# Kernel optimization log

Measured on AMD Instinct MI355X. Metric: run time of the kernel, lower is better.

Reference implementation:

```python
import jax, jax.numpy as jnp
from jax import lax
import numpy as np

EPS = 1e-6

def layer_norm(x, scale, bias):
    mu = jnp.mean(x, axis=-1, keepdims=True)
    var = jnp.var(x, axis=-1, keepdims=True)
    y = (x - mu) * lax.rsqrt(var + EPS)
    if scale is not None:
        y = y * scale
    if bias is not None:
        y = y + bias
    return y

def mha(keys, values, queries, mask, head_count):
    # keys/values: [B, K, E]; queries: [B, Q, E]; mask: [B, K] (1 = attend)
    B, Q, E = queries.shape
    d = E // head_count
    q = queries.reshape(B, Q, head_count, d) / jnp.asarray(d ** 0.5, queries.dtype)
    k = keys.reshape(B, -1, head_count, d)
    v = values.reshape(B, -1, head_count, d)
    bias = (1.0 - mask.astype(q.dtype)) * -1e12  # [B, K]
    w = jnp.einsum('bqhc,bkhc->bhqk', q, k) + bias[:, None, None, :]
    w = jax.nn.softmax(w, axis=-1)
    out = jnp.einsum('bhqk,bkhc->bqhc', w, v)
    return out.reshape(B, Q, E)

def setup_inputs() -> dict:
    key = jax.random.key(0)
    ks = jax.random.split(key, 16)
    B, T, E, G, I = 64, 64, 2048, 4096, 256
    s = 0.02
    inp = {
        'decoder_state': jax.random.normal(ks[0], (B, 1, E), jnp.float32),
        'encoder_state': jax.random.normal(ks[1], (B, T, E), jnp.float32),
        'attention_state': jnp.zeros((2 * B, I, E), jnp.float32),
        'attention_mask': jnp.ones((B, T), jnp.int32),
        'token_index': 100,
        # params
        'ln_pre_sa_b': jnp.zeros((E,), jnp.float32),
        'q_sa': s * jax.random.normal(ks[2], (E, E), jnp.float32),
        'k_sa': s * jax.random.normal(ks[3], (E, E), jnp.float32),
        'v_sa': s * jax.random.normal(ks[4], (E, E), jnp.float32),
        'o_sa': s * jax.random.normal(ks[5], (E, E), jnp.float32),
        'ln_sa_s': jnp.ones((E,), jnp.float32),
        'ln_sa_b': jnp.zeros((E,), jnp.float32),
        'ln_pre_ca_b': jnp.zeros((E,), jnp.float32),
        'q_ca': s * jax.random.normal(ks[6], (E, E), jnp.float32),
        'k_ca': s * jax.random.normal(ks[7], (E, E), jnp.float32),
        'v_ca': s * jax.random.normal(ks[8], (E, E), jnp.float32),
        'o_ca': s * jax.random.normal(ks[9], (E, E), jnp.float32),
        'ln_ca_s': jnp.ones((E,), jnp.float32),
        'ln_ca_b': jnp.zeros((E,), jnp.float32),
        'glu_ln0_b': jnp.zeros((E,), jnp.float32),
        'fc0_w': s * jax.random.normal(ks[10], (E, G), jnp.float32),
        'fc1_w': s * jax.random.normal(ks[11], (E, G), jnp.float32),
        'glu_ln1_s': jnp.ones((G,), jnp.float32),
        'glu_ln1_b': jnp.zeros((G,), jnp.float32),
        'fc2_w': s * jax.random.normal(ks[12], (G, E), jnp.float32),
    }
    return inp

IMAGE_TOKEN_COUNT = 256
HEAD_COUNT = 32

def reference(decoder_state, encoder_state, attention_state,
              ln_pre_sa_b, q_sa, k_sa, v_sa, o_sa, ln_sa_s, ln_sa_b,
              ln_pre_ca_b, q_ca, k_ca, v_ca, o_ca, ln_ca_s, ln_ca_b,
              glu_ln0_b, fc0_w, fc1_w, glu_ln1_s, glu_ln1_b, fc2_w,
              attention_mask, token_index):
    B = decoder_state.shape[0]
    # --- self attention (pre-norm, KV cache update) ---
    residual = decoder_state
    x = layer_norm(decoder_state, None, ln_pre_sa_b)
    self_mask = jnp.tile(jnp.arange(IMAGE_TOKEN_COUNT) < token_index + 1, (B, 1))
    keys = x @ k_sa
    values = x @ v_sa
    queries = x @ q_sa
    attention_state = lax.dynamic_update_slice(
        attention_state, jnp.concatenate([keys, values]).astype(jnp.float32),
        (0, token_index, 0))
    cached_k = attention_state[:B]
    cached_v = attention_state[B:]
    x = (mha(cached_k, cached_v, queries, self_mask, HEAD_COUNT) @ o_sa).astype(decoder_state.dtype)
    x = layer_norm(x, ln_sa_s, ln_sa_b)
    decoder_state = residual + x
    # --- cross attention ---
    residual = decoder_state
    x = layer_norm(decoder_state, None, ln_pre_ca_b)
    ek = encoder_state @ k_ca
    ev = encoder_state @ v_ca
    q = x @ q_ca
    x = mha(ek, ev, q, attention_mask, HEAD_COUNT) @ o_ca
    x = layer_norm(x, ln_ca_s, ln_ca_b)
    decoder_state = residual + x
    # --- GLU FFN ---
    residual = decoder_state
    z = layer_norm(decoder_state, None, glu_ln0_b)
    w = jax.nn.gelu(z @ fc0_w, approximate=False)
    v = z @ fc1_w
    z = layer_norm(w * v, glu_ln1_s, glu_ln1_b) @ fc2_w
    decoder_state = residual + z
    return decoder_state, attention_state
```

## Files before the change

kernel.cpp:

```cpp
#include <hip/hip_runtime.h>

#define Bb   64
#define Ee   2048
#define Tt   64
#define Gg   4096
#define Ii   256
#define Hh   32
#define Dd   64

using f32x4_t  = __attribute__((ext_vector_type(4))) float;
using bf16x8_t = __attribute__((ext_vector_type(8))) __bf16;

__device__ __forceinline__ unsigned short f2bf(float f) {
  unsigned u = __float_as_uint(f);
  u += 0x7FFFu + ((u >> 16) & 1u);
  return (unsigned short)(u >> 16);
}
__device__ __forceinline__ float ldkv(float v) { return v; }
__device__ __forceinline__ float ldkv(unsigned short v) {
  return __uint_as_float(((unsigned)v) << 16);
}
__device__ __forceinline__ float gelu_f(float x) {
  return 0.5f * x * (1.0f + erff(x * 0.70710678118654752f));
}

template <typename T> __device__ __forceinline__ float4 ld4(const T* p);
template <> __device__ __forceinline__ float4 ld4<float>(const float* p) {
  return *(const float4*)p;
}
template <> __device__ __forceinline__ float4 ld4<unsigned short>(const unsigned short* p) {
  ushort4 u = *(const ushort4*)p;
  return make_float4(ldkv(u.x), ldkv(u.y), ldkv(u.z), ldkv(u.w));
}

__global__ void copy_state_k(const float4* __restrict__ src, float4* __restrict__ dst,
                             const float4* __restrict__ kb, const float4* __restrict__ vb,
                             const int* __restrict__ tokp) {
  const int t = *tokp;
  const long n4 = (long)128 * Ii * (Ee / 4);
  long i = (long)blockIdx.x * blockDim.x + threadIdx.x;
  const long stride = (long)gridDim.x * blockDim.x;
  for (; i < n4; i += stride) {
    long row = i >> 9;
    int tt = (int)(row & (Ii - 1));
    float4 v;
    if (tt == t) {
      int bh  = (int)(row >> 8);
      int col = (int)(i & 511);
      const float4* s = (bh < Bb) ? kb : vb;
      v = s[(long)(bh & (Bb - 1)) * (Ee / 4) + col];
    } else {
      v = src[i];
    }
    dst[i] = v;
  }
}

__global__ void conv_bf16_k(const float4* __restrict__ in, unsigned short* __restrict__ out, long n4) {
  long i = (long)blockIdx.x * blockDim.x + threadIdx.x;
  long stride = (long)gridDim.x * blockDim.x;
  for (; i < n4; i += stride) {
    float4 f = in[i];
    ushort4 u;
    u.x = f2bf(f.x); u.y = f2bf(f.y); u.z = f2bf(f.z); u.w = f2bf(f.w);
    *(ushort4*)(out + i * 4) = u;
  }
}

__global__ void transpose_bf16_k(const float* __restrict__ W, unsigned short* __restrict__ Wt,
                                 int K, int N) {
  __shared__ unsigned short tile[64][65];
  int k0 = blockIdx.x * 64, n0 = blockIdx.y * 64;
  int c = threadIdx.x & 63;
  int r4 = threadIdx.x >> 6;
  #pragma unroll
  for (int i = 0; i < 16; i++) {
    int r = r4 + i * 4;
    tile[r][c] = f2bf(W[(long)(k0 + r) * N + n0 + c]);
  }
  __syncthreads();
  #pragma unroll
  for (int i = 0; i < 16; i++) {
    int r = r4 + i * 4;
    Wt[(long)(n0 + r) * K + k0 + c] = tile[c][r];
  }
}

template <bool GELU, bool HAS_SCALE, bool HAS_RES, bool DUAL>
__global__ void ln_k(const float4* __restrict__ in1, const float4* __restrict__ in2,
                     const float* __restrict__ scale, const float* __restrict__ bias,
                     const float4* __restrict__ res,
                     float4* __restrict__ out1, float4* __restrict__ out2) {
  const int row = blockIdx.x, tid = threadIdx.x;
  const int C = blockDim.x * 4;
  const long base = (long)row * blockDim.x + tid;

  float4 p = in1[base];
  if (GELU) {
    float4 vv = in2[base];
    p.x = gelu_f(p.x) * vv.x; p.y = gelu_f(p.y) * vv.y;
    p.z = gelu_f(p.z) * vv.z; p.w = gelu_f(p.w) * vv.w;
  }
  float s  = p.x + p.y + p.z + p.w;
  float s2 = p.x * p.x + p.y * p.y + p.z * p.z + p.w * p.w;

  __shared__ float rs[16], rs2[16];
  int lane = tid & 63, w = tid >> 6;
  #pragma unroll
  for (int o = 32; o; o >>= 1) { s += __shfl_down(s, o, 64); s2 += __shfl_down(s2, o, 64); }
  if (lane == 0) { rs[w] = s; rs2[w] = s2; }
  __syncthreads();
  if (tid == 0) {
    float ts = 0.f, ts2 = 0.f;
    int nw = blockDim.x >> 6;
    for (int i = 0; i < nw; i++) { ts += rs[i]; ts2 += rs2[i]; }
    float mu = ts / C;
    float var = ts2 / C - mu * mu;
    rs[0]  = mu;
    rs2[0] = rsqrtf(var + 1e-6f);
  }
  __syncthreads();
  const float mu = rs[0], rstd = rs2[0];

  float4 o;
  o.x = (p.x - mu) * rstd; o.y = (p.y - mu) * rstd;
  o.z = (p.z - mu) * rstd; o.w = (p.w - mu) * rstd;
  if (HAS_SCALE) {
    float4 sc4 = ((const float4*)scale)[tid];
    o.x *= sc4.x; o.y *= sc4.y; o.z *= sc4.z; o.w *= sc4.w;
  }
  float4 b4 = ((const float4*)bias)[tid];
  o.x += b4.x; o.y += b4.y; o.z += b4.z; o.w += b4.w;
  if (HAS_RES) {
    float4 r4 = res[base];
    o.x += r4.x; o.y += r4.y; o.z += r4.z; o.w += r4.w;
  }
  out1[base] = o;
  if (DUAL) out2[base] = o;
}

template <int NW>
__global__ __launch_bounds__(256)
void proj_k(const float* __restrict__ X,
            const float* __restrict__ W0, const float* __restrict__ W1,
            const float* __restrict__ W2,
            float* __restrict__ P, int K, int N) {
  __shared__ float Xs[64 * 64];
  const int nq = threadIdx.x & 31;
  const int m0 = (threadIdx.x >> 5) * 8;
  const int n  = blockIdx.x * 128 + nq * 4;
  const int kbase = blockIdx.y * 128;

  f32x4_t acc[NW][8];
  #pragma unroll
  for (int wsel = 0; wsel < NW; wsel++)
    #pragma unroll
    for (int i = 0; i < 8; i++) acc[wsel][i] = (f32x4_t){0.f, 0.f, 0.f, 0.f};

  for (int k0 = kbase; k0 < kbase + 128; k0 += 64) {
    __syncthreads();
    #pragma unroll
    for (int j = 0; j < 16; j++) {
      int e = threadIdx.x + j * 256;
      Xs[e] = X[(long)(e >> 6) * K + k0 + (e & 63)];
    }
    __syncthreads();
    #pragma unroll 4
    for (int kk = 0; kk < 64; kk++) {
      const long wrow = (long)(k0 + kk) * N + n;
      f32x4_t w4[NW];
      w4[0] = *(const f32x4_t*)(W0 + wrow);
      if (NW > 1) w4[1] = *(const f32x4_t*)(W1 + wrow);
      if (NW > 2) w4[2] = *(const f32x4_t*)(W2 + wrow);
      #pragma unroll
      for (int i = 0; i < 8; i++) {
        float xm = Xs[(m0 + i) * 64 + kk];
        #pragma unroll
        for (int wsel = 0; wsel < NW; wsel++) acc[wsel][i] += xm * w4[wsel];
      }
    }
  }
  float* base = P + (long)blockIdx.y * ((long)NW * 64 * N);
  #pragma unroll
  for (int wsel = 0; wsel < NW; wsel++) {
    #pragma unroll
    for (int i = 0; i < 8; i++) {
      *(f32x4_t*)(base + ((long)wsel * 64 + m0 + i) * N + n) = acc[wsel][i];
    }
  }
}

template <bool ACCUM>
__global__ void reduce_k(const float4* __restrict__ P, float4* __restrict__ Y,
                         int KB, long n4) {
  long i = (long)blockIdx.x * blockDim.x + threadIdx.x;
  if (i >= n4) return;
  float4 s = ACCUM ? Y[i] : make_float4(0.f, 0.f, 0.f, 0.f);
  for (int k = 0; k < KB; k++) {
    float4 p = P[(long)k * n4 + i];
    s.x += p.x; s.y += p.y; s.z += p.z; s.w += p.w;
  }
  Y[i] = s;
}

template <typename KVT>
__global__ void attn_k(const float* __restrict__ Q, const KVT* __restrict__ Kc,
                       const KVT* __restrict__ Vc, float* __restrict__ O,
                       const int* __restrict__ tokp, const int* __restrict__ maskp,
                       int L, long bstride, float scale) {
  const int b = blockIdx.x, h = blockIdx.y;
  const int lane = threadIdx.x;
  __shared__ float sc[256];
  const float* qp = Q + (long)b * Ee + h * Dd;
  const int n = tokp ? (*tokp + 1) : L;

  float mx = -3.0e38f;
  for (int pos = lane; pos < n; pos += 64) {
    bool valid = maskp ? (maskp[(long)b * L + pos] != 0) : true;
    float s = -1.0e30f;
    if (valid) {
      const KVT* kr = Kc + (long)b * bstride + (long)pos * Ee + h * Dd;
      float acc = 0.f;
      #pragma unroll
      for (int j = 0; j < 16; j++) {
        float4 kv = ld4(kr + j * 4);
        acc += qp[j*4+0]*kv.x + qp[j*4+1]*kv.y + qp[j*4+2]*kv.z + qp[j*4+3]*kv.w;
      }
      s = acc * scale;
    }
    sc[pos] = s;
    mx = fmaxf(mx, s);
  }
  __syncthreads();
  #pragma unroll
  for (int o = 32; o; o >>= 1) mx = fmaxf(mx, __shfl_down(mx, o, 64));
  mx = __shfl(mx, 0, 64);

  float sum = 0.f;
  for (int pos = lane; pos < n; pos += 64) {
    float e = expf(sc[pos] - mx);
    sc[pos] = e;
    sum += e;
  }
  __syncthreads();
  #pragma unroll
  for (int o = 32; o; o >>= 1) sum += __shfl_down(sum, o, 64);
  sum = __shfl(sum, 0, 64);
  const float inv = 1.0f / sum;

  const KVT* vbase = Vc + (long)b * bstride + h * Dd + lane;
  float acc = 0.f;
  int pos = 0;
  for (; pos + 8 <= n; pos += 8) {
    #pragma unroll
    for (int u = 0; u < 8; u++)
      acc += sc[pos + u] * ldkv(vbase[(long)(pos + u) * Ee]);
  }
  for (; pos < n; pos++) acc += sc[pos] * ldkv(vbase[(long)pos * Ee]);
  O[(long)b * Ee + h * Dd + lane] = acc * inv;
}

__global__ __launch_bounds__(256)
void gemm_bf16_k(const unsigned short* __restrict__ A, const unsigned short* __restrict__ Bt,
                 unsigned short* __restrict__ C, int M, int N, int K) {
  __shared__ unsigned short As[128 * 32];
  __shared__ unsigned short Bs[128 * 32];
  const int m0 = blockIdx.x * 128;
  const int n0 = blockIdx.y * 128;
  const int tid  = threadIdx.x;
  const int lane = tid & 63;
  const int wave = tid >> 6;
  const int wm = (wave >> 1) * 64;
  const int wn = (wave & 1) * 64;
  const int fr = lane & 15;
  const int fq = lane >> 4;

  const int r0 = tid >> 2;
  const int g0 = tid & 3;
  const int so1 = r0 * 32 + ((g0 ^ ((r0 >> 1) & 3)) * 8);
  const int so2 = so1 + 64 * 32;

  f32x4_t acc[4][4];
  const f32x4_t zero = {0.f, 0.f, 0.f, 0.f};
  #pragma unroll
  for (int i = 0; i < 4; i++)
    #pragma unroll
    for (int j = 0; j < 4; j++) acc[i][j] = zero;

  const long aR1 = (long)(m0 + r0) * K;
  const long aR2 = (long)(m0 + r0 + 64) * K;
  const long bR1 = (long)(n0 + r0) * K;
  const long bR2 = (long)(n0 + r0 + 64) * K;

  for (int k0 = 0; k0 < K; k0 += 32) {
    uint4 va1 = *(const uint4*)(A  + aR1 + k0 + g0 * 8);
    uint4 va2 = *(const uint4*)(A  + aR2 + k0 + g0 * 8);
    uint4 vb1 = *(const uint4*)(Bt + bR1 + k0 + g0 * 8);
    uint4 vb2 = *(const uint4*)(Bt + bR2 + k0 + g0 * 8);
    __syncthreads();
    *(uint4*)(As + so1) = va1;
    *(uint4*)(As + so2) = va2;
    *(uint4*)(Bs + so1) = vb1;
    *(uint4*)(Bs + so2) = vb2;
    __syncthreads();

    bf16x8_t af[4], bb[4];
    #pragma unroll
    for (int ms = 0; ms < 4; ms++) {
      int row = wm + ms * 16 + fr;
      af[ms] = __builtin_bit_cast(bf16x8_t,
               *(const uint4*)(As + row * 32 + ((fq ^ ((row >> 1) & 3)) * 8)));
    }
    #pragma unroll
    for (int ns = 0; ns < 4; ns++) {
      int row = wn + ns * 16 + fr;
      bb[ns] = __builtin_bit_cast(bf16x8_t,
               *(const uint4*)(Bs + row * 32 + ((fq ^ ((row >> 1) & 3)) * 8)));
    }
    #pragma unroll
    for (int ms = 0; ms < 4; ms++)
      #pragma unroll
      for (int ns = 0; ns < 4; ns++)
        acc[ms][ns] = __builtin_amdgcn_mfma_f32_16x16x32_bf16(af[ms], bb[ns], acc[ms][ns], 0, 0, 0);
  }

  #pragma unroll
  for (int ms = 0; ms < 4; ms++) {
    #pragma unroll
    for (int ns = 0; ns < 4; ns++) {
      int row = m0 + wm + ms * 16 + fq * 4;
      int col = n0 + wn + ns * 16 + fr;
      #pragma unroll
      for (int r = 0; r < 4; r++)
        C[(long)(row + r) * N + col] = f2bf(acc[ms][ns][r]);
    }
  }
}

extern "C" void kernel_launch(void* const* d_in, const int* in_sizes, int n_in,
                              void* d_out, int out_size, void* d_ws, size_t ws_size,
                              hipStream_t stream) {
  const float* dec    = (const float*)d_in[0];
  const float* enc    = (const float*)d_in[1];
  const float* astate = (const float*)d_in[2];
  const int*   amask  = (const int*)d_in[3];
  const int*   tokp   = (const int*)d_in[4];
  const float* ln_pre_sa_b = (const float*)d_in[5];
  const float* q_sa = (const float*)d_in[6];
  const float* k_sa = (const float*)d_in[7];
  const float* v_sa = (const float*)d_in[8];
  const float* o_sa = (const float*)d_in[9];
  const float* ln_sa_s = (const float*)d_in[10];
  const float* ln_sa_b = (const float*)d_in[11];
  const float* ln_pre_ca_b = (const float*)d_in[12];
  const float* q_ca = (const float*)d_in[13];
  const float* k_ca = (const float*)d_in[14];
  const float* v_ca = (const float*)d_in[15];
  const float* o_ca = (const float*)d_in[16];
  const float* ln_ca_s = (const float*)d_in[17];
  const float* ln_ca_b = (const float*)d_in[18];
  const float* glu_ln0_b = (const float*)d_in[19];
  const float* fc0 = (const float*)d_in[20];
  const float* fc1 = (const float*)d_in[21];
  const float* glu_ln1_s = (const float*)d_in[22];
  const float* glu_ln1_b = (const float*)d_in[23];
  const float* fc2 = (const float*)d_in[24];

  float* out_dec   = (float*)d_out;
  float* out_state = out_dec + (long)Bb * Ee;

  float* qb  = (float*)d_ws;
  float* kb  = qb  + 131072;
  float* vb  = kb  + 131072;
  float* ob  = vb  + 131072;
  float* q2  = ob  + 131072;
  float* ob2 = q2  + 131072;
  float* w0  = ob2 + 131072;
  float* v1  = w0  + 262144;
  float* x1  = v1  + 262144;
  float* ab  = x1  + 131072;
  float* ds2 = ab  + 131072;
  float* x3  = ds2 + 131072;
  float* cb  = x3  + 131072;
  float* ds3 = cb  + 131072;
  float* zb  = ds3 + 131072;
  float* wvn = zb  + 131072;
  unsigned short* ebf = (unsigned short*)(wvn + 262144);
  unsigned short* kt  = ebf + 8388608;
  unsigned short* vt  = kt  + 4194304;
  unsigned short* ekb = vt  + 4194304;
  unsigned short* evb = ekb + 8388608;
  float* arena = (float*)(evb + 8388608);

  conv_bf16_k<<<2048, 256, 0, stream>>>((const float4*)enc, ebf, (long)Bb * Tt * Ee / 4);
  transpose_bf16_k<<<dim3(32, 32), 256, 0, stream>>>(k_ca, kt, Ee, Ee);
  transpose_bf16_k<<<dim3(32, 32), 256, 0, stream>>>(v_ca, vt, Ee, Ee);
  gemm_bf16_k<<<dim3(32, 16), 256, 0, stream>>>(ebf, kt, ekb, 4096, Ee, Ee);
  gemm_bf16_k<<<dim3(32, 16), 256, 0, stream>>>(ebf, vt, evb, 4096, Ee, Ee);

  ln_k<false,false,false,false><<<Bb, 512, 0, stream>>>(
      (const float4*)dec, nullptr, nullptr, ln_pre_sa_b, nullptr, (float4*)x1, nullptr);
  proj_k<3><<<dim3(16, 16), 256, 0, stream>>>(x1, q_sa, k_sa, v_sa, arena, Ee, Ee);
  reduce_k<false><<<384, 256, 0, stream>>>((const float4*)arena, (float4*)qb, 16, 98304);
  copy_state_k<<<4096, 256, 0, stream>>>((const float4*)astate, (float4*)out_state,
                                         (const float4*)kb, (const float4*)vb, tokp);
  attn_k<float><<<dim3(Bb, Hh), 64, 0, stream>>>(qb, out_state,
      out_state + (long)Bb * Ii * Ee, ab, tokp, nullptr, Ii, (long)Ii * Ee, 0.125f);
  proj_k<1><<<dim3(16, 16), 256, 0, stream>>>(ab, o_sa, nullptr, nullptr, arena, Ee, Ee);
  reduce_k<false><<<128, 256, 0, stream>>>((const float4*)arena, (float4*)ob, 16, 32768);
  ln_k<false,true,true,false><<<Bb, 512, 0, stream>>>(
      (const float4*)ob, nullptr, ln_sa_s, ln_sa_b, (const float4*)dec, (float4*)ds2, nullptr);

  ln_k<false,false,false,false><<<Bb, 512, 0, stream>>>(
      (const float4*)ds2, nullptr, nullptr, ln_pre_ca_b, nullptr, (float4*)x3, nullptr);
  proj_k<1><<<dim3(16, 16), 256, 0, stream>>>(x3, q_ca, nullptr, nullptr, arena, Ee, Ee);
  reduce_k<false><<<128, 256, 0, stream>>>((const float4*)arena, (float4*)q2, 16, 32768);
  attn_k<unsigned short><<<dim3(Bb, Hh), 64, 0, stream>>>(q2, ekb, evb, cb,
      nullptr, amask, Tt, (long)Tt * Ee, 0.125f);
  proj_k<1><<<dim3(16, 16), 256, 0, stream>>>(cb, o_ca, nullptr, nullptr, arena, Ee, Ee);
  reduce_k<false><<<128, 256, 0, stream>>>((const float4*)arena, (float4*)ob2, 16, 32768);
  ln_k<false,true,true,true><<<Bb, 512, 0, stream>>>(
      (const float4*)ob2, nullptr, ln_ca_s, ln_ca_b, (const float4*)ds2,
      (float4*)ds3, (float4*)out_dec);

  ln_k<false,false,false,false><<<Bb, 512, 0, stream>>>(
      (const float4*)ds3, nullptr, nullptr, glu_ln0_b, nullptr, (float4*)zb, nullptr);
  proj_k<2><<<dim3(32, 16), 256, 0, stream>>>(zb, fc0, fc1, nullptr, arena, Ee, Gg);
  reduce_k<false><<<512, 256, 0, stream>>>((const float4*)arena, (float4*)w0, 16, 131072);
  ln_k<true,true,false,false><<<Bb, 1024, 0, stream>>>(
      (const float4*)w0, (const float4*)v1, glu_ln1_s, glu_ln1_b, nullptr, (float4*)wvn, nullptr);
  proj_k<1><<<dim3(16, 32), 256, 0, stream>>>(wvn, fc2, nullptr, nullptr, arena, Gg, Ee);
  reduce_k<true><<<128, 256, 0, stream>>>((const float4*)arena, (float4*)out_dec, 32, 32768);
}
```

Baseline: 1.067 ms.

## Fuse prep, split-K reductions and layernorms; merge dual bf16 GEMM with LDS-direct loads

Merges the encoder bf16 conversion and both weight transposes into one prep kernel. The K and V encoder GEMMs now run as a single launch that stages tiles with global_load_lds direct-to-LDS loads and no swizzle. Split-K reductions are folded into the state copy, the attention query load, and combined reduce+LN+residual+LN and reduce+GELU+LN kernels. The aim is to cut launch count and intermediate global round-trips, at the risk of LDS bank conflicts in the unswizzled GEMM and smaller per-block parallelism in the reductions.

```diff
diff --git a/kernel.cpp b/kernel.cpp
--- a/kernel.cpp
+++ b/kernel.cpp
@@ -23,6 +23,11 @@
 __device__ __forceinline__ float gelu_f(float x) {
   return 0.5f * x * (1.0f + erff(x * 0.70710678118654752f));
 }
+__device__ __forceinline__ void gld16(const void* g, void* l) {
+  __builtin_amdgcn_global_load_lds(
+      (const __attribute__((address_space(1))) unsigned int*)g,
+      (__attribute__((address_space(3))) unsigned int*)l, 16, 0, 0);
+}
 
 template <typename T> __device__ __forceinline__ float4 ld4(const T* p);
 template <> __device__ __forceinline__ float4 ld4<float>(const float* p) {
@@ -33,74 +38,115 @@
   return make_float4(ldkv(u.x), ldkv(u.y), ldkv(u.z), ldkv(u.w));
 }
 
-__global__ void copy_state_k(const float4* __restrict__ src, float4* __restrict__ dst,
-                             const float4* __restrict__ kb, const float4* __restrict__ vb,
-                             const int* __restrict__ tokp) {
-  const int t = *tokp;
-  const long n4 = (long)128 * Ii * (Ee / 4);
-  long i = (long)blockIdx.x * blockDim.x + threadIdx.x;
-  const long stride = (long)gridDim.x * blockDim.x;
-  for (; i < n4; i += stride) {
-    long row = i >> 9;
-    int tt = (int)(row & (Ii - 1));
-    float4 v;
-    if (tt == t) {
-      int bh  = (int)(row >> 8);
-      int col = (int)(i & 511);
-      const float4* s = (bh < Bb) ? kb : vb;
-      v = s[(long)(bh & (Bb - 1)) * (Ee / 4) + col];
-    } else {
-      v = src[i];
-    }
-    dst[i] = v;
-  }
-}
-
-__global__ void conv_bf16_k(const float4* __restrict__ in, unsigned short* __restrict__ out, long n4) {
-  long i = (long)blockIdx.x * blockDim.x + threadIdx.x;
-  long stride = (long)gridDim.x * blockDim.x;
-  for (; i < n4; i += stride) {
-    float4 f = in[i];
-    ushort4 u;
-    u.x = f2bf(f.x); u.y = f2bf(f.y); u.z = f2bf(f.z); u.w = f2bf(f.w);
-    *(ushort4*)(out + i * 4) = u;
-  }
-}
-
-__global__ void transpose_bf16_k(const float* __restrict__ W, unsigned short* __restrict__ Wt,
-                                 int K, int N) {
-  __shared__ unsigned short tile[64][65];
-  int k0 = blockIdx.x * 64, n0 = blockIdx.y * 64;
-  int c = threadIdx.x & 63;
-  int r4 = threadIdx.x >> 6;
-  #pragma unroll
-  for (int i = 0; i < 16; i++) {
-    int r = r4 + i * 4;
-    tile[r][c] = f2bf(W[(long)(k0 + r) * N + n0 + c]);
-  }
-  __syncthreads();
-  #pragma unroll
-  for (int i = 0; i < 16; i++) {
-    int r = r4 + i * 4;
-    Wt[(long)(n0 + r) * K + k0 + c] = tile[c][r];
-  }
-}
-
-template <bool GELU, bool HAS_SCALE, bool HAS_RES, bool DUAL>
-__global__ void ln_k(const float4* __restrict__ in1, const float4* __restrict__ in2,
-                     const float* __restrict__ scale, const float* __restrict__ bias,
-                     const float4* __restrict__ res,
-                     float4* __restrict__ out1, float4* __restrict__ out2) {
+__global__ void prep_k(const float* __restrict__ enc, unsigned short* __restrict__ ebf,
+                       const float* __restrict__ Wk, unsigned short* __restrict__ kt,
+                       const float* __restrict__ Wv, unsigned short* __restrict__ vt) {
+  int bid = blockIdx.x;
+  if (bid < 2048) {
+    const float* W = (bid < 1024) ? Wk : Wv;
+    unsigned short* Wt = (bid < 1024) ? kt : vt;
+    int ti = bid & 1023;
+    __shared__ unsigned short tile[64][65];
+    int k0 = (ti & 31) * 64, n0 = (ti >> 5) * 64;
+    int c = threadIdx.x & 63;
+    int r4 = threadIdx.x >> 6;
+    #pragma unroll
+    for (int i = 0; i < 16; i++) {
+      int r = r4 + i * 4;
+      tile[r][c] = f2bf(W[(long)(k0 + r) * Ee + n0 + c]);
+    }
+    __syncthreads();
+    #pragma unroll
+    for (int i = 0; i < 16; i++) {
+      int r = r4 + i * 4;
+      Wt[(long)(n0 + r) * Ee + k0 + c] = tile[c][r];
+    }
+  } else {
+    long i = (long)(bid - 2048) * 256 + threadIdx.x;
+    const long n4 = (long)Bb * Tt * Ee / 4;
+    for (; i < n4; i += 2048L * 256) {
+      float4 f = ((const float4*)enc)[i];
+      ushort4 u;
+      u.x = f2bf(f.x); u.y = f2bf(f.y); u.z = f2bf(f.z); u.w = f2bf(f.w);
+      *(ushort4*)(ebf + i * 4) = u;
+    }
+  }
+}
+
+__global__ __launch_bounds__(256)
+void gemm2_k(const unsigned short* __restrict__ A,
+             const unsigned short* __restrict__ B0t, const unsigned short* __restrict__ B1t,
+             unsigned short* __restrict__ C0, unsigned short* __restrict__ C1,
+             int M, int N, int K) {
+  __shared__ __align__(16) unsigned short As[4096];
+  __shared__ __align__(16) unsigned short Bs[2][2048];
+  const int m0 = blockIdx.x * 128;
+  const int n0 = blockIdx.y * 64;
+  const int tid  = threadIdx.x;
+  const int lane = tid & 63;
+  const int wave = tid >> 6;
+  const int out  = wave >> 1;
+  const int wm   = (wave & 1) * 64;
+  const int fr = lane & 15;
+  const int fq = lane >> 4;
+
+  f32x4_t acc[4][4];
+  const f32x4_t zero = {0.f, 0.f, 0.f, 0.f};
+  #pragma unroll
+  for (int i = 0; i < 4; i++)
+    #pragma unroll
+    for (int j = 0; j < 4; j++) acc[i][j] = zero;
+
+  for (int k0 = 0; k0 < K; k0 += 32) {
+    __syncthreads();
+    #pragma unroll
+    for (int p = 0; p < 2; p++) {
+      int c = p * 4 + wave;
+      int kg = c >> 1, mh = c & 1;
+      gld16(A + (long)(m0 + mh * 64 + lane) * K + k0 + kg * 8,
+            &As[kg * 1024 + mh * 512]);
+    }
+    gld16(B0t + (long)(n0 + lane) * K + k0 + wave * 8, &Bs[0][wave * 512]);
+    gld16(B1t + (long)(n0 + lane) * K + k0 + wave * 8, &Bs[1][wave * 512]);
+    __syncthreads();
+
+    bf16x8_t af[4], bf_[4];
+    #pragma unroll
+    for (int ms = 0; ms < 4; ms++)
+      af[ms] = __builtin_bit_cast(bf16x8_t,
+               *(const uint4*)&As[fq * 1024 + (wm + ms * 16 + fr) * 8]);
+    #pragma unroll
+    for (int ns = 0; ns < 4; ns++)
+      bf_[ns] = __builtin_bit_cast(bf16x8_t,
+               *(const uint4*)&Bs[out][fq * 512 + (ns * 16 + fr) * 8]);
+    #pragma unroll
+    for (int ms = 0; ms < 4; ms++)
+      #pragma unroll
+      for (int ns = 0; ns < 4; ns++)
+        acc[ms][ns] = __builtin_amdgcn_mfma_f32_16x16x32_bf16(af[ms], bf_[ns], acc[ms][ns], 0, 0, 0);
+  }
+
+  unsigned short* C = out ? C1 : C0;
+  #pragma unroll
+  for (int ms = 0; ms < 4; ms++) {
+    #pragma unroll
+    for (int ns = 0; ns < 4; ns++) {
+      int row = m0 + wm + ms * 16 + fq * 4;
+      int col = n0 + ns * 16 + fr;
+      #pragma unroll
+      for (int r = 0; r < 4; r++)
+        C[(long)(row + r) * N + col] = f2bf(acc[ms][ns][r]);
+    }
+  }
+}
+
+__global__ void ln_k(const float4* __restrict__ in1, const float* __restrict__ bias,
+                     float4* __restrict__ out1) {
   const int row = blockIdx.x, tid = threadIdx.x;
   const int C = blockDim.x * 4;
   const long base = (long)row * blockDim.x + tid;
 
   float4 p = in1[base];
-  if (GELU) {
-    float4 vv = in2[base];
-    p.x = gelu_f(p.x) * vv.x; p.y = gelu_f(p.y) * vv.y;
-    p.z = gelu_f(p.z) * vv.z; p.w = gelu_f(p.w) * vv.w;
-  }
   float s  = p.x + p.y + p.z + p.w;
   float s2 = p.x * p.x + p.y * p.y + p.z * p.z + p.w * p.w;
 
@@ -115,28 +161,124 @@
     int nw = blockDim.x >> 6;
     for (int i = 0; i < nw; i++) { ts += rs[i]; ts2 += rs2[i]; }
     float mu = ts / C;
-    float var = ts2 / C - mu * mu;
     rs[0]  = mu;
-    rs2[0] = rsqrtf(var + 1e-6f);
+    rs2[0] = rsqrtf(ts2 / C - mu * mu + 1e-6f);
   }
   __syncthreads();
   const float mu = rs[0], rstd = rs2[0];
-
+  float4 b4 = ((const float4*)bias)[tid];
   float4 o;
-  o.x = (p.x - mu) * rstd; o.y = (p.y - mu) * rstd;
-  o.z = (p.z - mu) * rstd; o.w = (p.w - mu) * rstd;
-  if (HAS_SCALE) {
-    float4 sc4 = ((const float4*)scale)[tid];
-    o.x *= sc4.x; o.y *= sc4.y; o.z *= sc4.z; o.w *= sc4.w;
-  }
-  float4 b4 = ((const float4*)bias)[tid];
-  o.x += b4.x; o.y += b4.y; o.z += b4.z; o.w += b4.w;
-  if (HAS_RES) {
-    float4 r4 = res[base];
-    o.x += r4.x; o.y += r4.y; o.z += r4.z; o.w += r4.w;
-  }
+  o.x = (p.x - mu) * rstd + b4.x; o.y = (p.y - mu) * rstd + b4.y;
+  o.z = (p.z - mu) * rstd + b4.z; o.w = (p.w - mu) * rstd + b4.w;
   out1[base] = o;
-  if (DUAL) out2[base] = o;
+}
+
+template <bool DUAL>
+__global__ void redln2_k(const float4* __restrict__ P, long ks4, int KB,
+                         const float* __restrict__ s1, const float* __restrict__ b1,
+                         const float4* __restrict__ res, const float* __restrict__ b2,
+                         float4* __restrict__ o_res, float4* __restrict__ o_res2,
+                         float4* __restrict__ o_ln) {
+  const int row = blockIdx.x, tid = threadIdx.x;
+  const int C = blockDim.x * 4;
+  const long base = (long)row * blockDim.x + tid;
+
+  float4 p = make_float4(0.f, 0.f, 0.f, 0.f);
+  for (int k = 0; k < KB; k++) {
+    float4 q = P[(long)k * ks4 + base];
+    p.x += q.x; p.y += q.y; p.z += q.z; p.w += q.w;
+  }
+
+  __shared__ float rs[16], rs2[16];
+  const int lane = tid & 63, w = tid >> 6;
+  const int nw = blockDim.x >> 6;
+  float s = p.x + p.y + p.z + p.w;
+  float s2 = p.x * p.x + p.y * p.y + p.z * p.z + p.w * p.w;
+  #pragma unroll
+  for (int o = 32; o; o >>= 1) { s += __shfl_down(s, o, 64); s2 += __shfl_down(s2, o, 64); }
+  if (lane == 0) { rs[w] = s; rs2[w] = s2; }
+  __syncthreads();
+  if (tid == 0) {
+    float ts = 0.f, ts2 = 0.f;
+    for (int i = 0; i < nw; i++) { ts += rs[i]; ts2 += rs2[i]; }
+    float mu = ts / C;
+    rs[0] = mu; rs2[0] = rsqrtf(ts2 / C - mu * mu + 1e-6f);
+  }
+  __syncthreads();
+  const float mu1 = rs[0], rstd1 = rs2[0];
+  float4 sc = ((const float4*)s1)[tid];
+  float4 bb = ((const float4*)b1)[tid];
+  float4 r4 = res[base];
+  float4 y;
+  y.x = (p.x - mu1) * rstd1 * sc.x + bb.x + r4.x;
+  y.y = (p.y - mu1) * rstd1 * sc.y + bb.y + r4.y;
+  y.z = (p.z - mu1) * rstd1 * sc.z + bb.z + r4.z;
+  y.w = (p.w - mu1) * rstd1 * sc.w + bb.w + r4.w;
+  o_res[base] = y;
+  if (DUAL) o_res2[base] = y;
+  s = y.x + y.y + y.z + y.w;
+  s2 = y.x * y.x + y.y * y.y + y.z * y.z + y.w * y.w;
+  #pragma unroll
+  for (int o = 32; o; o >>= 1) { s += __shfl_down(s, o, 64); s2 += __shfl_down(s2, o, 64); }
+  __syncthreads();
+  if (lane == 0) { rs[w] = s; rs2[w] = s2; }
+  __syncthreads();
+  if (tid == 0) {
+    float ts = 0.f, ts2 = 0.f;
+    for (int i = 0; i < nw; i++) { ts += rs[i]; ts2 += rs2[i]; }
+    float mu = ts / C;
+    rs[0] = mu; rs2[0] = rsqrtf(ts2 / C - mu * mu + 1e-6f);
+  }
+  __syncthreads();
+  const float mu2 = rs[0], rstd2 = rs2[0];
+  float4 b24 = ((const float4*)b2)[tid];
+  float4 z;
+  z.x = (y.x - mu2) * rstd2 + b24.x; z.y = (y.y - mu2) * rstd2 + b24.y;
+  z.z = (y.z - mu2) * rstd2 + b24.z; z.w = (y.w - mu2) * rstd2 + b24.w;
+  o_ln[base] = z;
+}
+
+__global__ void redln_gelu_k(const float4* __restrict__ P, long ks4, int KB, long off2,
+                             const float* __restrict__ scale, const float* __restrict__ bias,
+                             float4* __restrict__ out) {
+  const int row = blockIdx.x, tid = threadIdx.x;
+  const int C = blockDim.x * 4;
+  const long base = (long)row * blockDim.x + tid;
+
+  float4 a = make_float4(0.f, 0.f, 0.f, 0.f), b = a;
+  for (int k = 0; k < KB; k++) {
+    float4 q = P[(long)k * ks4 + base];
+    a.x += q.x; a.y += q.y; a.z += q.z; a.w += q.w;
+    float4 r = P[(long)k * ks4 + off2 + base];
+    b.x += r.x; b.y += r.y; b.z += r.z; b.w += r.w;
+  }
+  float4 p;
+  p.x = gelu_f(a.x) * b.x; p.y = gelu_f(a.y) * b.y;
+  p.z = gelu_f(a.z) * b.z; p.w = gelu_f(a.w) * b.w;
+
+  float s  = p.x + p.y + p.z + p.w;
+  float s2 = p.x * p.x + p.y * p.y + p.z * p.z + p.w * p.w;
+  __shared__ float rs[16], rs2[16];
+  int lane = tid & 63, w = tid >> 6;
+  #pragma unroll
+  for (int o = 32; o; o >>= 1) { s += __shfl_down(s, o, 64); s2 += __shfl_down(s2, o, 64); }
+  if (lane == 0) { rs[w] = s; rs2[w] = s2; }
+  __syncthreads();
+  if (tid == 0) {
+    float ts = 0.f, ts2 = 0.f;
+    int nw = blockDim.x >> 6;
+    for (int i = 0; i < nw; i++) { ts += rs[i]; ts2 += rs2[i]; }
+    float mu = ts / C;
+    rs[0] = mu; rs2[0] = rsqrtf(ts2 / C - mu * mu + 1e-6f);
+  }
+  __syncthreads();
+  const float mu = rs[0], rstd = rs2[0];
+  float4 sc4 = ((const float4*)scale)[tid];
+  float4 b4  = ((const float4*)bias)[tid];
+  float4 o;
+  o.x = (p.x - mu) * rstd * sc4.x + b4.x; o.y = (p.y - mu) * rstd * sc4.y + b4.y;
+  o.z = (p.z - mu) * rstd * sc4.z + b4.z; o.w = (p.w - mu) * rstd * sc4.w + b4.w;
+  out[base] = o;
 }
 
 template <int NW>
@@ -182,20 +324,17 @@
   }
   float* base = P + (long)blockIdx.y * ((long)NW * 64 * N);
   #pragma unroll
-  for (int wsel = 0; wsel < NW; wsel++) {
-    #pragma unroll
-    for (int i = 0; i < 8; i++) {
+  for (int wsel = 0; wsel < NW; wsel++)
+    #pragma unroll
+    for (int i = 0; i < 8; i++)
       *(f32x4_t*)(base + ((long)wsel * 64 + m0 + i) * N + n) = acc[wsel][i];
-    }
-  }
-}
-
-template <bool ACCUM>
-__global__ void reduce_k(const float4* __restrict__ P, float4* __restrict__ Y,
-                         int KB, long n4) {
+}
+
+__global__ void reduce_acc_k(const float4* __restrict__ P, float4* __restrict__ Y,
+                             int KB, long n4) {
   long i = (long)blockIdx.x * blockDim.x + threadIdx.x;
   if (i >= n4) return;
-  float4 s = ACCUM ? Y[i] : make_float4(0.f, 0.f, 0.f, 0.f);
+  float4 s = Y[i];
   for (int k = 0; k < KB; k++) {
     float4 p = P[(long)k * n4 + i];
     s.x += p.x; s.y += p.y; s.z += p.z; s.w += p.w;
@@ -203,16 +342,68 @@
   Y[i] = s;
 }
 
+__global__ void copyred_k(const float4* __restrict__ src, float4* __restrict__ dst,
+                          const float4* __restrict__ arena, float4* __restrict__ qb,
+                          const int* __restrict__ tokp) {
+  const int t = *tokp;
+  const int bid = blockIdx.x;
+  if (bid < 128) {
+    long i = (long)bid * 256 + threadIdx.x;
+    float4 s = make_float4(0.f, 0.f, 0.f, 0.f);
+    for (int k = 0; k < 16; k++) {
+      float4 p = arena[(long)k * 98304 + i];
+      s.x += p.x; s.y += p.y; s.z += p.z; s.w += p.w;
+    }
+    qb[i] = s;
+    return;
+  }
+  const long n4 = (long)128 * Ii * (Ee / 4);
+  long i = (long)(bid - 128) * 256 + threadIdx.x;
+  const long stride = (long)(gridDim.x - 128) * 256;
+  for (; i < n4; i += stride) {
+    long row = i >> 9;
+    int tt = (int)(row & (Ii - 1));
+    float4 v;
+    if (tt == t) {
+      int bh  = (int)(row >> 8);
+      int col = (int)(i & 511);
+      long off = (bh < Bb) ? (32768L + (long)bh * 512 + col)
+                           : (65536L + (long)(bh - Bb) * 512 + col);
+      v = make_float4(0.f, 0.f, 0.f, 0.f);
+      for (int k = 0; k < 16; k++) {
+        float4 p = arena[(long)k * 98304 + off];
+        v.x += p.x; v.y += p.y; v.z += p.z; v.w += p.w;
+      }
+    } else {
+      v = src[i];
+    }
+    dst[i] = v;
+  }
+}
+
 template <typename KVT>
-__global__ void attn_k(const float* __restrict__ Q, const KVT* __restrict__ Kc,
-                       const KVT* __restrict__ Vc, float* __restrict__ O,
+__global__ void attn_k(const float* __restrict__ Q, const float* __restrict__ qred, long qks,
+                       const KVT* __restrict__ Kc, const KVT* __restrict__ Vc,
+                       float* __restrict__ O,
                        const int* __restrict__ tokp, const int* __restrict__ maskp,
                        int L, long bstride, float scale) {
   const int b = blockIdx.x, h = blockIdx.y;
   const int lane = threadIdx.x;
   __shared__ float sc[256];
-  const float* qp = Q + (long)b * Ee + h * Dd;
+  __shared__ float sq[64];
   const int n = tokp ? (*tokp + 1) : L;
+
+  const float* qp;
+  if (qred) {
+    float s = 0.f;
+    long e = (long)b * Ee + h * Dd + lane;
+    for (int k = 0; k < 16; k++) s += qred[(long)k * qks + e];
+    sq[lane] = s;
+    __syncthreads();
+    qp = sq;
+  } else {
+    qp = Q + (long)b * Ee + h * Dd;
+  }
 
   float mx = -3.0e38f;
   for (int pos = lane; pos < n; pos += 64) {
@@ -258,83 +449,6 @@
   }
   for (; pos < n; pos++) acc += sc[pos] * ldkv(vbase[(long)pos * Ee]);
   O[(long)b * Ee + h * Dd + lane] = acc * inv;
-}
-
-__global__ __launch_bounds__(256)
-void gemm_bf16_k(const unsigned short* __restrict__ A, const unsigned short* __restrict__ Bt,
-                 unsigned short* __restrict__ C, int M, int N, int K) {
-  __shared__ unsigned short As[128 * 32];
-  __shared__ unsigned short Bs[128 * 32];
-  const int m0 = blockIdx.x * 128;
-  const int n0 = blockIdx.y * 128;
-  const int tid  = threadIdx.x;
-  const int lane = tid & 63;
-  const int wave = tid >> 6;
-  const int wm = (wave >> 1) * 64;
-  const int wn = (wave & 1) * 64;
-  const int fr = lane & 15;
-  const int fq = lane >> 4;
-
-  const int r0 = tid >> 2;
-  const int g0 = tid & 3;
-  const int so1 = r0 * 32 + ((g0 ^ ((r0 >> 1) & 3)) * 8);
-  const int so2 = so1 + 64 * 32;
-
-  f32x4_t acc[4][4];
-  const f32x4_t zero = {0.f, 0.f, 0.f, 0.f};
-  #pragma unroll
-  for (int i = 0; i < 4; i++)
-    #pragma unroll
-    for (int j = 0; j < 4; j++) acc[i][j] = zero;
-
-  const long aR1 = (long)(m0 + r0) * K;
-  const long aR2 = (long)(m0 + r0 + 64) * K;
-  const long bR1 = (long)(n0 + r0) * K;
-  const long bR2 = (long)(n0 + r0 + 64) * K;
-
-  for (int k0 = 0; k0 < K; k0 += 32) {
-    uint4 va1 = *(const uint4*)(A  + aR1 + k0 + g0 * 8);
-    uint4 va2 = *(const uint4*)(A  + aR2 + k0 + g0 * 8);
-    uint4 vb1 = *(const uint4*)(Bt + bR1 + k0 + g0 * 8);
-    uint4 vb2 = *(const uint4*)(Bt + bR2 + k0 + g0 * 8);
-    __syncthreads();
-    *(uint4*)(As + so1) = va1;
-    *(uint4*)(As + so2) = va2;
-    *(uint4*)(Bs + so1) = vb1;
-    *(uint4*)(Bs + so2) = vb2;
-    __syncthreads();
-
-    bf16x8_t af[4], bb[4];
-    #pragma unroll
-    for (int ms = 0; ms < 4; ms++) {
-      int row = wm + ms * 16 + fr;
-      af[ms] = __builtin_bit_cast(bf16x8_t,
-               *(const uint4*)(As + row * 32 + ((fq ^ ((row >> 1) & 3)) * 8)));
-    }
-    #pragma unroll
-    for (int ns = 0; ns < 4; ns++) {
-      int row = wn + ns * 16 + fr;
-      bb[ns] = __builtin_bit_cast(bf16x8_t,
-               *(const uint4*)(Bs + row * 32 + ((fq ^ ((row >> 1) & 3)) * 8)));
-    }
-    #pragma unroll
-    for (int ms = 0; ms < 4; ms++)
-      #pragma unroll
-      for (int ns = 0; ns < 4; ns++)
-        acc[ms][ns] = __builtin_amdgcn_mfma_f32_16x16x32_bf16(af[ms], bb[ns], acc[ms][ns], 0, 0, 0);
-  }
-
-  #pragma unroll
-  for (int ms = 0; ms < 4; ms++) {
-    #pragma unroll
-    for (int ns = 0; ns < 4; ns++) {
-      int row = m0 + wm + ms * 16 + fq * 4;
-      int col = n0 + wn + ns * 16 + fr;
-      #pragma unroll
-      for (int r = 0; r < 4; r++)
-        C[(long)(row + r) * N + col] = f2bf(acc[ms][ns][r]);
-    }
-  }
 }
 
 extern "C" void kernel_launch(void* const* d_in, const int* in_sizes, int n_in,
@@ -369,16 +483,9 @@
   float* out_dec   = (float*)d_out;
   float* out_state = out_dec + (long)Bb * Ee;
 
-  float* qb  = (float*)d_ws;
-  float* kb  = qb  + 131072;
-  float* vb  = kb  + 131072;
-  float* ob  = vb  + 131072;
-  float* q2  = ob  + 131072;
-  float* ob2 = q2  + 131072;
-  float* w0  = ob2 + 131072;
-  float* v1  = w0  + 262144;
-  float* x1  = v1  + 262144;
-  float* ab  = x1  + 131072;
+  float* x1  = (float*)d_ws;
+  float* qb  = x1  + 131072;
+  float* ab  = qb  + 131072;
   float* ds2 = ab  + 131072;
   float* x3  = ds2 + 131072;
   float* cb  = x3  + 131072;
@@ -392,43 +499,31 @@
   unsigned short* evb = ekb + 8388608;
   float* arena = (float*)(evb + 8388608);
 
-  conv_bf16_k<<<2048, 256, 0, stream>>>((const float4*)enc, ebf, (long)Bb * Tt * Ee / 4);
-  transpose_bf16_k<<<dim3(32, 32), 256, 0, stream>>>(k_ca, kt, Ee, Ee);
-  transpose_bf16_k<<<dim3(32, 32), 256, 0, stream>>>(v_ca, vt, Ee, Ee);
-  gemm_bf16_k<<<dim3(32, 16), 256, 0, stream>>>(ebf, kt, ekb, 4096, Ee, Ee);
-  gemm_bf16_k<<<dim3(32, 16), 256, 0, stream>>>(ebf, vt, evb, 4096, Ee, Ee);
-
-  ln_k<false,false,false,false><<<Bb, 512, 0, stream>>>(
-      (const float4*)dec, nullptr, nullptr, ln_pre_sa_b, nullptr, (float4*)x1, nullptr);
+  prep_k<<<4096, 256, 0, stream>>>(enc, ebf, k_ca, kt, v_ca, vt);
+  gemm2_k<<<dim3(32, 32), 256, 0, stream>>>(ebf, kt, vt, ekb, evb, 4096, Ee, Ee);
+
+  ln_k<<<Bb, 512, 0, stream>>>((const float4*)dec, ln_pre_sa_b, (float4*)x1);
   proj_k<3><<<dim3(16, 16), 256, 0, stream>>>(x1, q_sa, k_sa, v_sa, arena, Ee, Ee);
-  reduce_k<false><<<384, 256, 0, stream>>>((const float4*)arena, (float4*)qb, 16, 98304);
-  copy_state_k<<<4096, 256, 0, stream>>>((const float4*)astate, (float4*)out_state,
-                                         (const float4*)kb, (const float4*)vb, tokp);
-  attn_k<float><<<dim3(Bb, Hh), 64, 0, stream>>>(qb, out_state,
+  copyred_k<<<8320, 256, 0, stream>>>((const float4*)astate, (float4*)out_state,
+                                      (const float4*)arena, (float4*)qb, tokp);
+  attn_k<float><<<dim3(Bb, Hh), 64, 0, stream>>>(qb, nullptr, 0, out_state,
       out_state + (long)Bb * Ii * Ee, ab, tokp, nullptr, Ii, (long)Ii * Ee, 0.125f);
   proj_k<1><<<dim3(16, 16), 256, 0, stream>>>(ab, o_sa, nullptr, nullptr, arena, Ee, Ee);
-  reduce_k<false><<<128, 256, 0, stream>>>((const float4*)arena, (float4*)ob, 16, 32768);
-  ln_k<false,true,true,false><<<Bb, 512, 0, stream>>>(
-      (const float4*)ob, nullptr, ln_sa_s, ln_sa_b, (const float4*)dec, (float4*)ds2, nullptr);
-
-  ln_k<false,false,false,false><<<Bb, 512, 0, stream>>>(
-      (const float4*)ds2, nullptr, nullptr, ln_pre_ca_b, nullptr, (float4*)x3, nullptr);
+  redln2_k<false><<<Bb, 512, 0, stream>>>((const float4*)arena, 32768, 16,
+      ln_sa_s, ln_sa_b, (const float4*)dec, ln_pre_ca_b,
+      (float4*)ds2, nullptr, (float4*)x3);
+
   proj_k<1><<<dim3(16, 16), 256, 0, stream>>>(x3, q_ca, nullptr, nullptr, arena, Ee, Ee);
-  reduce_k<false><<<128, 256, 0, stream>>>((const float4*)arena, (float4*)q2, 16, 32768);
-  attn_k<unsigned short><<<dim3(Bb, Hh), 64, 0, stream>>>(q2, ekb, evb, cb,
-      nullptr, amask, Tt, (long)Tt * Ee, 0.125f);
+  attn_k<unsigned short><<<dim3(Bb, Hh), 64, 0, stream>>>(nullptr, arena, 131072,
+      ekb, evb, cb, nullptr, amask, Tt, (long)Tt * Ee, 0.125f);
   proj_k<1><<<dim3(16, 16), 256, 0, stream>>>(cb, o_ca, nullptr, nullptr, arena, Ee, Ee);
-  reduce_k<false><<<128, 256, 0, stream>>>((const float4*)arena, (float4*)ob2, 16, 32768);
-  ln_k<false,true,true,true><<<Bb, 512, 0, stream>>>(
-      (const float4*)ob2, nullptr, ln_ca_s, ln_ca_b, (const float4*)ds2,
-      (float4*)ds3, (float4*)out_dec);
-
-  ln_k<false,false,false,false><<<Bb, 512, 0, stream>>>(
-      (const float4*)ds3, nullptr, nullptr, glu_ln0_b, nullptr, (float4*)zb, nullptr);
+  redln2_k<true><<<Bb, 512, 0, stream>>>((const float4*)arena, 32768, 16,
+      ln_ca_s, ln_ca_b, (const float4*)ds2, glu_ln0_b,
+      (float4*)ds3, (float4*)out_dec, (float4*)zb);
+
   proj_k<2><<<dim3(32, 16), 256, 0, stream>>>(zb, fc0, fc1, nullptr, arena, Ee, Gg);
-  reduce_k<false><<<512, 256, 0, stream>>>((const float4*)arena, (float4*)w0, 16, 131072);
-  ln_k<true,true,false,false><<<Bb, 1024, 0, stream>>>(
-      (const float4*)w0, (const float4*)v1, glu_ln1_s, glu_ln1_b, nullptr, (float4*)wvn, nullptr);
+  redln_gelu_k<<<Bb, 1024, 0, stream>>>((const float4*)arena, 131072, 16, 65536,
+      glu_ln1_s, glu_ln1_b, (float4*)wvn);
   proj_k<1><<<dim3(16, 32), 256, 0, stream>>>(wvn, fc2, nullptr, nullptr, arena, Gg, Ee);
-  reduce_k<true><<<128, 256, 0, stream>>>((const float4*)arena, (float4*)out_dec, 32, 32768);
-}
+  reduce_acc_k<<<128, 256, 0, stream>>>((const float4*)arena, (float4*)out_dec, 32, 32768);
+}
```

Result: slower. 1.127 ms (+5.6%).
